# Kernel tuning notes

Hardware: AMD Instinct MI355X
Metric: run time of the kernel (lower is better)

Reference implementation:

```python
import jax, jax.numpy as jnp
import numpy as np

B, CIN, COUT, T, H, W, NH = 8, 16, 16, 32, 16, 16, 4
DIN = CIN * H * W    # 4096
DOUT = COUT * H * W  # 4096
DH = DOUT // NH      # 1024


def conv3d(x, w, b, pad):
    y = jax.lax.conv_general_dilated(
        x, w, window_strides=(1, 1, 1), padding=((pad, pad),) * 3,
        dimension_numbers=('NCDHW', 'OIDHW', 'NCDHW'))
    return y + b[None, :, None, None, None]


def instance_norm(x, eps=1e-5):
    # InstanceNorm3d default: no affine, normalize per (B,C) over (T,H,W)
    mu = x.mean(axis=(2, 3, 4), keepdims=True)
    var = ((x - mu) ** 2).mean(axis=(2, 3, 4), keepdims=True)
    return (x - mu) * jax.lax.rsqrt(var + eps)


def slstm(x, Wg, bg, Rg):
    # x: (B,T,D). Wg: (4,D,D) input weights [i,f,z,o]; bg: (4,D);
    # Rg: (NH,4,DH,DH) block-diagonal per-head recurrent weights.
    Bb, Tt, D = x.shape
    Gx = jnp.einsum('btd,god->btgo', x, Wg) + bg  # (B,T,4,D)

    def step(carry, gx):
        h, c, n, m = carry
        hh = h.reshape(Bb, NH, DH)
        gh = jnp.einsum('bhd,hgod->bhgo', hh, Rg)          # (B,NH,4,DH)
        pre = gx + gh.transpose(0, 2, 1, 3).reshape(Bb, 4, D)
        i_pre, f_pre, z_pre, o_pre = pre[:, 0], pre[:, 1], pre[:, 2], pre[:, 3]
        # stabilized exponential gating (xLSTM sLSTM)
        m_new = jnp.maximum(f_pre + m, i_pre)
        i = jnp.exp(i_pre - m_new)
        f = jnp.exp(f_pre + m - m_new)
        c = f * c + i * jnp.tanh(z_pre)
        n = f * n + i
        h = jax.nn.sigmoid(o_pre) * c / n
        return (h, c, n, m_new), h

    init = tuple(jnp.zeros((Bb, D), x.dtype) for _ in range(4))
    _, hs = jax.lax.scan(step, init, Gx.transpose(1, 0, 2, 3))  # hs: (T,B,D)
    return hs.transpose(1, 0, 2)


def setup_inputs():
    key = jax.random.key(0)
    ks = jax.random.split(key, 8)
    s = 0.02
    return {
        'x': jax.random.normal(ks[0], (B, CIN, T, H, W), jnp.float32),
        'c1_w': jax.random.normal(ks[1], (COUT, CIN, 3, 3, 3), jnp.float32) * 0.05,
        'c1_b': jnp.zeros((COUT,), jnp.float32),
        'c2_w': jax.random.normal(ks[2], (COUT, COUT, 3, 3, 3), jnp.float32) * 0.05,
        'c2_b': jnp.zeros((COUT,), jnp.float32),
        'c3_w': jax.random.normal(ks[3], (COUT, COUT, 3, 3, 3), jnp.float32) * 0.05,
        'c3_b': jnp.zeros((COUT,), jnp.float32),
        'pre_w': jax.random.normal(ks[4], (DOUT, DIN), jnp.float32) * s,
        'pre_b': jnp.zeros((DOUT,), jnp.float32),
        'lstm_W': jax.random.normal(ks[5], (4, DOUT, DOUT), jnp.float32) * s,
        'lstm_b': jnp.zeros((4, DOUT), jnp.float32),
        'lstm_R': jax.random.normal(ks[6], (NH, 4, DH, DH), jnp.float32) * s,
        'attn_w': jax.random.normal(ks[7], (1, 2 * COUT), jnp.float32) * 0.05,
        'attn_b': jnp.zeros((1,), jnp.float32),
    }


def reference(x, c1_w, c1_b, c2_w, c2_b, c3_w, c3_b, pre_w, pre_b,
              lstm_W, lstm_b, lstm_R, attn_w, attn_b):
    # conv3d branch: conv -> IN -> relu -> conv -> relu -> conv -> relu
    y = jax.nn.relu(instance_norm(conv3d(x, c1_w, c1_b, 1)))
    y = jax.nn.relu(conv3d(y, c2_w, c2_b, 1))
    out3d = jax.nn.relu(conv3d(y, c3_w, c3_b, 1))
    # sLSTM branch
    xs = x.transpose(0, 2, 1, 3, 4).reshape(B, T, DIN)
    xs = xs @ pre_w.T + pre_b
    hs = slstm(xs, lstm_W, lstm_b, lstm_R)                 # (B,T,DOUT)
    s_out = hs.reshape(B, T, COUT, H, W).transpose(0, 2, 1, 3, 4)
    # attention-gated fusion: cat -> 1x1x1 conv -> sigmoid -> weighted sum
    comb = jnp.concatenate([s_out, out3d], axis=1)         # (B,2*COUT,T,H,W)
    alpha = jax.nn.sigmoid(jnp.einsum('bcthw,oc->bothw', comb, attn_w)
                           + attn_b[None, :, None, None, None])
    return alpha * out3d + (1 - alpha) * s_out
```

## Files before the change

kernel.cpp:

```cpp
#include <hip/hip_runtime.h>
#include <hip/hip_bf16.h>
#include <cstddef>

#define BB   8
#define CIN  16
#define COUT 16
#define TT   32
#define HH   16
#define WW   16
#define DIN  4096
#define DOUT 4096
#define NH   4
#define DH   1024
#define SPAT 8192
#define NSEQ 256

typedef __attribute__((ext_vector_type(8))) short  bf16x8;
typedef __attribute__((ext_vector_type(4))) float  f32x4;
typedef __attribute__((ext_vector_type(4))) unsigned short us4;
typedef __attribute__((ext_vector_type(4))) int    i32x4;
typedef unsigned short ushort_t;
typedef unsigned long long u64_t;

static __device__ __forceinline__ ushort_t f2bf(float f) {
    union { float f; unsigned u; } v; v.f = f;
    unsigned r = (v.u + 0x7fffu + ((v.u >> 16) & 1u)) >> 16;
    return (ushort_t)r;
}
static __device__ __forceinline__ float bf2f(ushort_t u) {
    union { unsigned u; float f; } v; v.u = ((unsigned)u) << 16;
    return v.f;
}

__global__ void setup_kernel(const float* __restrict__ x, ushort_t* __restrict__ xt,
                             const float* __restrict__ w1, const float* __restrict__ w2,
                             const float* __restrict__ w3,
                             float* __restrict__ cw1, float* __restrict__ cw2,
                             float* __restrict__ cw3, int* __restrict__ flags) {
    int bid = blockIdx.x;
    if (bid < 1024) {
        int idx = bid * 256 + threadIdx.x;
        int n = idx >> 10, k4 = (idx & 1023) * 4;
        int b = n >> 5, t = n & 31, c = k4 >> 8, hw = k4 & 255;
        f32x4 f = *(const f32x4*)&x[(((size_t)(b * CIN + c) * TT + t)) * 256 + hw];
        us4 o;
        #pragma unroll
        for (int i = 0; i < 4; ++i) o[i] = f2bf(f[i]);
        *(us4*)&xt[(size_t)n * DIN + k4] = o;
    } else if (bid < 1105) {
        int i = (bid - 1024) * 256 + threadIdx.x;
        if (i < 3 * 6912) {
            int set = i / 6912, j = i - set * 6912;
            const float* w = (set == 0) ? w1 : (set == 1) ? w2 : w3;
            float* cw      = (set == 0) ? cw1 : (set == 1) ? cw2 : cw3;
            int o = j & 15, r = j >> 4;
            int k = r % 27, ci = r / 27;
            cw[j] = w[(size_t)(o * CIN + ci) * 27 + k];
        }
    } else {
        int j = (bid - 1105) * 256 + threadIdx.x;
        ((i32x4*)flags)[j] = (i32x4){0, 0, 0, 0};
    }
}

template<int BN, int BK, bool OUT_BF16, bool ADD_BIAS>
__global__ __launch_bounds__(256, 2)
void mfma_gemm_kernel(const ushort_t* __restrict__ A, const float* __restrict__ B,
                      const float* __restrict__ bias, void* __restrict__ C,
                      int N, int K) {
    constexpr int NF  = BN / 16;
    constexpr int TPR = 256 / BN;
    constexpr int FPT = BK / TPR;
    constexpr int RPI = 512 / BK;
    constexpr int LPR = 64 / RPI;
    __shared__ ushort_t Al[2][256][BK];
    __shared__ ushort_t Bl[2][BN][BK];
    int tid  = threadIdx.x;
    int lane = tid & 63;
    int wv   = tid >> 6;
    int n0 = blockIdx.x * BN;
    int ksp = K / gridDim.y;
    int kS  = blockIdx.y * ksp;

    f32x4 acc[4][NF];
    #pragma unroll
    for (int i = 0; i < 4; ++i)
        #pragma unroll
        for (int j = 0; j < NF; ++j) acc[i][j] = (f32x4){0.f, 0.f, 0.f, 0.f};

    auto stageA = [&](int buf, int k0) {
        #pragma unroll
        for (int q = 0; q < BK / 8; ++q) {
            int rbase = wv * 64 + q * RPI;
            int row = rbase + lane / LPR;
            const ushort_t* g = A + (size_t)row * K + k0 + (lane % LPR) * 8;
            __builtin_amdgcn_global_load_lds(
                (const __attribute__((address_space(1))) void*)g,
                (__attribute__((address_space(3))) void*)&Al[buf][rbase][0],
                16, 0, 0);
        }
    };
    auto stageB = [&](int buf, int k0) {
        int r  = tid / TPR;
        int cs = (tid % TPR) * FPT;
        const float* g = B + (size_t)(n0 + r) * K + k0 + cs;
        #pragma unroll
        for (int q = 0; q < FPT / 4; ++q) {
            f32x4 f = *(const f32x4*)(g + q * 4);
            us4 pk;
            #pragma unroll
            for (int e = 0; e < 4; ++e) pk[e] = f2bf(f[e]);
            *(us4*)&Bl[buf][r][cs + q * 4] = pk;
        }
    };
    auto compute = [&](int buf) {
        #pragma unroll
        for (int ks = 0; ks < BK / 32; ++ks) {
            bf16x8 af[4], bfr[NF];
            #pragma unroll
            for (int i = 0; i < 4; ++i)
                af[i] = *(const bf16x8*)&Al[buf][wv * 64 + i * 16 + (lane & 15)][ks * 32 + (lane >> 4) * 8];
            #pragma unroll
            for (int j = 0; j < NF; ++j)
                bfr[j] = *(const bf16x8*)&Bl[buf][j * 16 + (lane & 15)][ks * 32 + (lane >> 4) * 8];
            #pragma unroll
            for (int i = 0; i < 4; ++i)
                #pragma unroll
                for (int j = 0; j < NF; ++j)
                    acc[i][j] = __builtin_amdgcn_mfma_f32_16x16x32_bf16(af[i], bfr[j], acc[i][j], 0, 0, 0);
        }
    };

    stageA(0, kS); stageB(0, kS);
    __syncthreads();
    int nk = ksp / BK;
    int cur = 0;
    for (int t = 0; t < nk; ++t) {
        if (t + 1 < nk) { stageA(cur ^ 1, kS + (t + 1) * BK); stageB(cur ^ 1, kS + (t + 1) * BK); }
        compute(cur);
        __syncthreads();
        cur ^= 1;
    }

    size_t cofs = (size_t)blockIdx.y * 256 * N;
    #pragma unroll
    for (int i = 0; i < 4; ++i) {
        int row = wv * 64 + i * 16 + (lane >> 4) * 4;
        #pragma unroll
        for (int j = 0; j < NF; ++j) {
            int col = n0 + j * 16 + (lane & 15);
            float bv = ADD_BIAS ? bias[col] : 0.f;
            #pragma unroll
            for (int r = 0; r < 4; ++r) {
                float v = acc[i][j][r] + bv;
                if constexpr (OUT_BF16) ((ushort_t*)C)[cofs + (size_t)(row + r) * N + col] = f2bf(v);
                else                    ((float*)C)[cofs + (size_t)(row + r) * N + col] = v;
            }
        }
    }
}

#define GXPS ((size_t)NSEQ * 4 * DOUT)

__global__ __launch_bounds__(256, 1)
void lstm_persist_kernel(const float* __restrict__ R,
                         const float* __restrict__ Gx,
                         const float* __restrict__ lstm_b,
                         unsigned* __restrict__ hfr,
                         int* __restrict__ flags) {
    __shared__ ushort_t Rl[4][32][64 * 8];
    __shared__ float gh_p[4][4][16][8];

    int tid  = threadIdx.x;
    int lane = tid & 63;
    int w    = tid >> 6;
    int head = blockIdx.x >> 6;
    int oc   = blockIdx.x & 63;

    #pragma unroll 4
    for (int n = 0; n < 64; ++n) {
        int g = n >> 4, r = n & 15;
        const float* src = R + ((size_t)((head * 4 + g) * DH + oc * 16 + r)) * DH + tid * 4;
        f32x4 f = *(const f32x4*)src;
        int k0 = tid * 4;
        int ks = k0 >> 5;
        int kI = (k0 >> 3) & 3;
        int e8 = k0 & 7;
        union { ushort_t u[4]; u64_t q; } pk;
        #pragma unroll
        for (int e = 0; e < 4; ++e) pk.u[e] = f2bf(f[e]);
        *(u64_t*)&Rl[g][ks][((kI << 4) | r) * 8 + e8] = pk.q;
    }

    int arow = lane & 15;
    int part = arow >> 3;
    int bb   = arow & 7;
    int kseg = lane >> 4;

    int gb  = tid >> 4;
    int gol = tid & 15;
    int gd  = head * DH + oc * 16 + gol;
    int o_h = oc * 16 + gol;
    unsigned hslot = ((unsigned)head * 32 + (o_h >> 5)) * 256 + gb * 32 + (o_h & 31);
    float c_r = 0.f, n_r = 0.f, m_r = 0.f;
    float lb0 = 0.f, lb1 = 0.f, lb2 = 0.f, lb3 = 0.f;
    if (tid < 128) {
        lb0 = lstm_b[gd];
        lb1 = lstm_b[DOUT + gd];
        lb2 = lstm_b[2 * DOUT + gd];
        lb3 = lstm_b[3 * DOUT + gd];
    }

    __syncthreads();

    for (int t = 0; t < TT; ++t) {
        float gx0 = lb0, gx1 = lb1, gx2 = lb2, gx3 = lb3;
        if (tid < 128) {
            size_t gxoff = ((size_t)(gb * TT + t)) * (4 * DOUT) + gd;
            #pragma unroll
            for (int p = 0; p < 4; ++p) {
                const float* gp = Gx + p * GXPS + gxoff;
                gx0 += gp[0];
                gx1 += gp[DOUT];
                gx2 += gp[2 * DOUT];
                gx3 += gp[3 * DOUT];
            }
        }

        if (t > 0) {
            const int* fl = flags + (((t - 1) * 4 + head) << 6);
            for (;;) {
                int v = __hip_atomic_load(fl + lane, __ATOMIC_RELAXED,
                                          __HIP_MEMORY_SCOPE_AGENT);
                if (__all(v != 0)) break;
            }

            const u64_t* hb = (const u64_t*)hfr
                + ((((size_t)(t - 1) * 4 + head) * 32) * 256 + bb * 32 + kseg * 8) / 2;
            bf16x8 hf[8];
            #pragma unroll
            for (int j = 0; j < 8; ++j) {
                const u64_t* p = hb + (size_t)(w * 8 + j) * 128;
                union { ushort_t u[8]; bf16x8 v; } fr;
                #pragma unroll
                for (int e2 = 0; e2 < 4; ++e2) {
                    u64_t q = __hip_atomic_load(p + e2, __ATOMIC_RELAXED,
                                                __HIP_MEMORY_SCOPE_AGENT);
                    unsigned q0 = (unsigned)q, q1 = (unsigned)(q >> 32);
                    fr.u[e2 * 2]     = part ? (ushort_t)(q0 >> 16) : (ushort_t)(q0 & 0xffffu);
                    fr.u[e2 * 2 + 1] = part ? (ushort_t)(q1 >> 16) : (ushort_t)(q1 & 0xffffu);
                }
                hf[j] = fr.v;
            }

            f32x4 acc[4];
            #pragma unroll
            for (int g = 0; g < 4; ++g) acc[g] = (f32x4){0.f, 0.f, 0.f, 0.f};
            #pragma unroll
            for (int g = 0; g < 4; ++g)
                #pragma unroll
                for (int j = 0; j < 8; ++j) {
                    bf16x8 a = *(const bf16x8*)&Rl[g][w * 8 + j][lane * 8];
                    acc[g] = __builtin_amdgcn_mfma_f32_16x16x32_bf16(a, hf[j], acc[g], 0, 0, 0);
                }
            #pragma unroll
            for (int g = 0; g < 4; ++g)
                #pragma unroll
                for (int r = 0; r < 4; ++r)
                    acc[g][r] += __shfl_xor(acc[g][r], 8, 64);
            if (part == 0) {
                int orow0 = kseg * 4;
                #pragma unroll
                for (int g = 0; g < 4; ++g)
                    #pragma unroll
                    for (int r = 0; r < 4; ++r)
                        gh_p[w][g][orow0 + r][bb] = acc[g][r];
            }
        } else {
            for (int i = tid; i < 4 * 4 * 16 * 8; i += 256)
                ((float*)gh_p)[i] = 0.f;
        }
        __syncthreads();

        if (tid < 128) {
            float ip = gx0 +
                gh_p[0][0][gol][gb] + gh_p[1][0][gol][gb] + gh_p[2][0][gol][gb] + gh_p[3][0][gol][gb];
            float fp = gx1 +
                gh_p[0][1][gol][gb] + gh_p[1][1][gol][gb] + gh_p[2][1][gol][gb] + gh_p[3][1][gol][gb];
            float zp = gx2 +
                gh_p[0][2][gol][gb] + gh_p[1][2][gol][gb] + gh_p[2][2][gol][gb] + gh_p[3][2][gol][gb];
            float op = gx3 +
                gh_p[0][3][gol][gb] + gh_p[1][3][gol][gb] + gh_p[2][3][gol][gb] + gh_p[3][3][gol][gb];
            float mn = fmaxf(fp + m_r, ip);
            float iv = __expf(ip - mn);
            float fv = __expf(fp + m_r - mn);
            float zc = fminf(fmaxf(zp, -9.f), 9.f);
            float th = 1.f - 2.f / (__expf(2.f * zc) + 1.f);
            c_r = fv * c_r + iv * th;
            n_r = fv * n_r + iv;
            float sig = 1.f / (1.f + __expf(-op));
            float hv = sig * c_r / n_r;
            m_r = mn;
            unsigned hi = f2bf(hv);
            unsigned lo = f2bf(hv - bf2f((ushort_t)hi));
            __hip_atomic_store(&hfr[(size_t)t * 32768 + hslot],
                               hi | (lo << 16),
                               __ATOMIC_RELAXED, __HIP_MEMORY_SCOPE_AGENT);
        }
        __syncthreads();
        if (tid == 0)
            __hip_atomic_store(&flags[((t * 4 + head) << 6) + oc], 1,
                               __ATOMIC_RELAXED, __HIP_MEMORY_SCOPE_AGENT);
    }
}

template<bool NORM, bool PSUM>
__global__ __launch_bounds__(256)
void conv3d_kernel(const float* __restrict__ in, const float* __restrict__ cw,
                   const float* __restrict__ bias, const float* __restrict__ stats,
                   float* __restrict__ out, float* __restrict__ psum, int relu) {
    __shared__ float xin[CIN][3][256];
    int blk = blockIdx.x;
    int b = blk >> 6, t = (blk >> 1) & 31, half = blk & 1;
    int tid = threadIdx.x;

    for (int i = tid; i < CIN * 3 * 256; i += 256) {
        int hw = i & 255, r = i >> 8;
        int kt = r % 3, ci = r / 3;
        int tt = t + kt - 1;
        float v = 0.f;
        if ((unsigned)tt < TT) {
            v = in[((size_t)(b * CIN + ci) * TT + tt) * 256 + hw];
            if constexpr (NORM) {
                float mu = stats[(b * CIN + ci) * 2];
                float rs = stats[(b * CIN + ci) * 2 + 1];
                v = fmaxf((v - mu) * rs, 0.f);
            }
        }
        xin[ci][kt][hw] = v;
    }
    __syncthreads();

    int h = tid >> 4, wx = tid & 15;
    f32x4 a0 = *(const f32x4*)&bias[half * 8];
    f32x4 a1 = *(const f32x4*)&bias[half * 8 + 4];

    for (int ci = 0; ci < CIN; ++ci) {
        #pragma unroll
        for (int kt = 0; kt < 3; ++kt) {
            #pragma unroll
            for (int kh = 0; kh < 3; ++kh) {
                int h2 = h + kh - 1;
                bool vh = (unsigned)h2 < HH;
                int h2c = vh ? h2 : 0;
                #pragma unroll
                for (int kw = 0; kw < 3; ++kw) {
                    int w2 = wx + kw - 1;
                    bool v = vh && ((unsigned)w2 < WW);
                    int w2c = ((unsigned)w2 < WW) ? w2 : 0;
                    float xv = xin[ci][kt][h2c * 16 + w2c];
                    xv = v ? xv : 0.f;
                    const float* wp = cw + (size_t)(ci * 27 + kt * 9 + kh * 3 + kw) * 16 + half * 8;
                    f32x4 w0 = *(const f32x4*)(wp);
                    f32x4 w1 = *(const f32x4*)(wp + 4);
                    a0 += xv * w0; a1 += xv * w1;
                }
            }
        }
    }
    float accs[8];
    #pragma unroll
    for (int i = 0; i < 4; ++i) { accs[i] = a0[i]; accs[4 + i] = a1[i]; }
    #pragma unroll
    for (int o = 0; o < 8; ++o) {
        float v = accs[o];
        if (relu) v = fmaxf(v, 0.f);
        out[((size_t)(b * COUT + half * 8 + o) * TT + t) * 256 + tid] = v;
    }

    if constexpr (PSUM) {
        __syncthreads();
        float* sm = (float*)xin;
        int wv = tid >> 6;
        #pragma unroll
        for (int o = 0; o < 8; ++o) {
            float s = accs[o];
            float q = accs[o] * accs[o];
            #pragma unroll
            for (int m = 1; m < 64; m <<= 1) {
                s += __shfl_xor(s, m, 64);
                q += __shfl_xor(q, m, 64);
            }
            if ((tid & 63) == 0) { sm[wv * 16 + o * 2] = s; sm[wv * 16 + o * 2 + 1] = q; }
        }
        __syncthreads();
        if (tid < 16) {
            int o = tid >> 1, which = tid & 1;
            float v = sm[o * 2 + which] + sm[16 + o * 2 + which]
                    + sm[32 + o * 2 + which] + sm[48 + o * 2 + which];
            psum[((((size_t)(b * 32 + t) * 2 + half) * 8 + o) * 2) + which] = v;
        }
    }
}

__global__ void inorm_stats_kernel(const float* __restrict__ psum, float* __restrict__ stats) {
    int tid = threadIdx.x;
    if (tid < 128) {
        int b = tid >> 4, c = tid & 15;
        int half = c >> 3, ch = c & 7;
        float sum = 0.f, sq = 0.f;
        for (int t = 0; t < TT; ++t) {
            size_t base = (((size_t)(b * 32 + t) * 2 + half) * 8 + ch) * 2;
            sum += psum[base];
            sq  += psum[base + 1];
        }
        float mu = sum / (float)SPAT;
        float var = sq / (float)SPAT - mu * mu;
        stats[(b * CIN + c) * 2]     = mu;
        stats[(b * CIN + c) * 2 + 1] = rsqrtf(var + 1e-5f);
    }
}

__global__ void combine_kernel(const unsigned* __restrict__ hfr,
                               const float* __restrict__ out3d,
                               const float* __restrict__ attn_w,
                               const float* __restrict__ attn_b,
                               float* __restrict__ out) {
    int idx = blockIdx.x * 256 + threadIdx.x;
    int hw = idx & 255;
    int t  = (idx >> 8) & 31;
    int b  = idx >> 13;
    float dot = attn_b[0];
    float sv[16], ov[16];
    #pragma unroll
    for (int ch = 0; ch < 16; ++ch) {
        int d = ch * 256 + hw;
        int head = d >> 10, o_h = d & 1023;
        size_t slot = (size_t)t * 32768 + (size_t)head * 8192
                    + (o_h >> 5) * 256 + b * 32 + (o_h & 31);
        unsigned v32 = hfr[slot];
        float s = bf2f((ushort_t)(v32 & 0xffffu)) + bf2f((ushort_t)(v32 >> 16));
        float o3 = out3d[(((size_t)(b * COUT + ch) * TT + t)) * 256 + hw];
        sv[ch] = s; ov[ch] = o3;
        dot += attn_w[ch] * s + attn_w[16 + ch] * o3;
    }
    float alpha = 1.f / (1.f + expf(-dot));
    #pragma unroll
    for (int ch = 0; ch < 16; ++ch) {
        out[(((size_t)(b * COUT + ch) * TT + t)) * 256 + hw] =
            alpha * ov[ch] + (1.f - alpha) * sv[ch];
    }
}

extern "C" void kernel_launch(void* const* d_in, const int* in_sizes, int n_in,
                              void* d_out, int out_size, void* d_ws, size_t ws_size,
                              hipStream_t stream) {
    const float* x      = (const float*)d_in[0];
    const float* c1_w   = (const float*)d_in[1];
    const float* c1_b   = (const float*)d_in[2];
    const float* c2_w   = (const float*)d_in[3];
    const float* c2_b   = (const float*)d_in[4];
    const float* c3_w   = (const float*)d_in[5];
    const float* c3_b   = (const float*)d_in[6];
    const float* pre_w  = (const float*)d_in[7];
    const float* pre_b  = (const float*)d_in[8];
    const float* lstm_W = (const float*)d_in[9];
    const float* lstm_b = (const float*)d_in[10];
    const float* lstm_R = (const float*)d_in[11];
    const float* attn_w = (const float*)d_in[12];
    const float* attn_b = (const float*)d_in[13];
    float* out = (float*)d_out;

    float* wsf = (float*)d_ws;
    float* y1    = wsf;
    float* y2    = y1 + 1048576;
    float* out3d = y2 + 1048576;
    float* Gx    = out3d + 1048576;
    float* cw1   = Gx + 4 * 4194304;
    float* cw2   = cw1 + 6912;
    float* cw3   = cw2 + 6912;
    float* stats = cw3 + 6912;
    float* psum  = stats + 256;
    float* pad   = psum + 8192;
    ushort_t* xt   = (ushort_t*)(pad + 64);
    ushort_t* xs2b = xt + 1048576;
    unsigned* hfr  = (unsigned*)(xs2b + 1048576);
    int*     flags = (int*)(hfr + 1048576);

    setup_kernel<<<1113, 256, 0, stream>>>(x, xt, c1_w, c2_w, c3_w, cw1, cw2, cw3, flags);

    conv3d_kernel<false, true><<<512, 256, 0, stream>>>(x, cw1, c1_b, nullptr, y1, psum, 0);
    inorm_stats_kernel<<<1, 256, 0, stream>>>(psum, stats);
    conv3d_kernel<true, false><<<512, 256, 0, stream>>>(y1, cw2, c2_b, stats, y2, nullptr, 1);
    conv3d_kernel<false, false><<<512, 256, 0, stream>>>(y2, cw3, c3_b, nullptr, out3d, nullptr, 1);

    mfma_gemm_kernel<16, 64, true, true><<<dim3(DOUT / 16, 1), 256, 0, stream>>>(
        xt, pre_w, pre_b, xs2b, DOUT, DIN);
    mfma_gemm_kernel<32, 64, false, false><<<dim3(4 * DOUT / 32, 4), 256, 0, stream>>>(
        xs2b, lstm_W, nullptr, Gx, 4 * DOUT, DOUT);

    lstm_persist_kernel<<<256, 256, 0, stream>>>(lstm_R, Gx, lstm_b, hfr, flags);

    combine_kernel<<<256, 256, 0, stream>>>(hfr, out3d, attn_w, attn_b, out);
}
```

Baseline: 603.4 us.

## Co-schedule conv blocks with GEMM blocks in fused kernels and halve Gx split-K

```diff
diff --git a/kernel.cpp b/kernel.cpp
--- a/kernel.cpp
+++ b/kernel.cpp
@@ -64,23 +64,22 @@
 }
 
 template<int BN, int BK, bool OUT_BF16, bool ADD_BIAS>
-__global__ __launch_bounds__(256, 2)
-void mfma_gemm_kernel(const ushort_t* __restrict__ A, const float* __restrict__ B,
-                      const float* __restrict__ bias, void* __restrict__ C,
-                      int N, int K) {
+__device__ __forceinline__
+void gemm_body(char* smem, int bx, int by, int nsplit,
+               const ushort_t* __restrict__ A, const float* __restrict__ B,
+               const float* __restrict__ bias, void* __restrict__ C,
+               int N, int K) {
     constexpr int NF  = BN / 16;
     constexpr int TPR = 256 / BN;
     constexpr int FPT = BK / TPR;
-    constexpr int RPI = 512 / BK;
-    constexpr int LPR = 64 / RPI;
-    __shared__ ushort_t Al[2][256][BK];
-    __shared__ ushort_t Bl[2][BN][BK];
+    ushort_t* Al = (ushort_t*)smem;
+    ushort_t* Bl = Al + 2 * 256 * BK;
     int tid  = threadIdx.x;
     int lane = tid & 63;
     int wv   = tid >> 6;
-    int n0 = blockIdx.x * BN;
-    int ksp = K / gridDim.y;
-    int kS  = blockIdx.y * ksp;
+    int n0 = bx * BN;
+    int ksp = K / nsplit;
+    int kS  = by * ksp;
 
     f32x4 acc[4][NF];
     #pragma unroll
@@ -90,13 +89,13 @@
 
     auto stageA = [&](int buf, int k0) {
         #pragma unroll
-        for (int q = 0; q < BK / 8; ++q) {
-            int rbase = wv * 64 + q * RPI;
-            int row = rbase + lane / LPR;
-            const ushort_t* g = A + (size_t)row * K + k0 + (lane % LPR) * 8;
+        for (int q = 0; q < 8; ++q) {
+            int rbase = wv * 64 + q * 8;
+            int row = rbase + (lane >> 3);
+            const ushort_t* g = A + (size_t)row * K + k0 + (lane & 7) * 8;
             __builtin_amdgcn_global_load_lds(
                 (const __attribute__((address_space(1))) void*)g,
-                (__attribute__((address_space(3))) void*)&Al[buf][rbase][0],
+                (__attribute__((address_space(3))) void*)&Al[(buf * 256 + rbase) * BK],
                 16, 0, 0);
         }
     };
@@ -110,7 +109,7 @@
             us4 pk;
             #pragma unroll
             for (int e = 0; e < 4; ++e) pk[e] = f2bf(f[e]);
-            *(us4*)&Bl[buf][r][cs + q * 4] = pk;
+            *(us4*)&Bl[(buf * BN + r) * BK + cs + q * 4] = pk;
         }
     };
     auto compute = [&](int buf) {
@@ -119,10 +118,10 @@
             bf16x8 af[4], bfr[NF];
             #pragma unroll
             for (int i = 0; i < 4; ++i)
-                af[i] = *(const bf16x8*)&Al[buf][wv * 64 + i * 16 + (lane & 15)][ks * 32 + (lane >> 4) * 8];
+                af[i] = *(const bf16x8*)&Al[(buf * 256 + wv * 64 + i * 16 + (lane & 15)) * BK + ks * 32 + (lane >> 4) * 8];
             #pragma unroll
             for (int j = 0; j < NF; ++j)
-                bfr[j] = *(const bf16x8*)&Bl[buf][j * 16 + (lane & 15)][ks * 32 + (lane >> 4) * 8];
+                bfr[j] = *(const bf16x8*)&Bl[(buf * BN + j * 16 + (lane & 15)) * BK + ks * 32 + (lane >> 4) * 8];
             #pragma unroll
             for (int i = 0; i < 4; ++i)
                 #pragma unroll
@@ -142,7 +141,7 @@
         cur ^= 1;
     }
 
-    size_t cofs = (size_t)blockIdx.y * 256 * N;
+    size_t cofs = (size_t)by * 256 * N;
     #pragma unroll
     for (int i = 0; i < 4; ++i) {
         int row = wv * 64 + i * 16 + (lane >> 4) * 4;
@@ -157,6 +156,147 @@
                 else                    ((float*)C)[cofs + (size_t)(row + r) * N + col] = v;
             }
         }
+    }
+}
+
+template<bool NORM, bool PSUM>
+__device__ __forceinline__
+void conv_body(char* smem, int blk,
+               const float* __restrict__ in, const float* __restrict__ cw,
+               const float* __restrict__ bias, const float* __restrict__ stats,
+               float* __restrict__ out, float* __restrict__ psum, int relu) {
+    float* xin = (float*)smem;
+    int b = blk >> 6, t = (blk >> 1) & 31, half = blk & 1;
+    int tid = threadIdx.x;
+
+    for (int i = tid; i < CIN * 3 * 256; i += 256) {
+        int hw = i & 255, r = i >> 8;
+        int kt = r % 3, ci = r / 3;
+        int tt = t + kt - 1;
+        float v = 0.f;
+        if ((unsigned)tt < TT) {
+            v = in[((size_t)(b * CIN + ci) * TT + tt) * 256 + hw];
+            if constexpr (NORM) {
+                float mu = stats[(b * CIN + ci) * 2];
+                float rs = stats[(b * CIN + ci) * 2 + 1];
+                v = fmaxf((v - mu) * rs, 0.f);
+            }
+        }
+        xin[(ci * 3 + kt) * 256 + hw] = v;
+    }
+    __syncthreads();
+
+    int h = tid >> 4, wx = tid & 15;
+    f32x4 a0 = *(const f32x4*)&bias[half * 8];
+    f32x4 a1 = *(const f32x4*)&bias[half * 8 + 4];
+
+    for (int ci = 0; ci < CIN; ++ci) {
+        #pragma unroll
+        for (int kt = 0; kt < 3; ++kt) {
+            #pragma unroll
+            for (int kh = 0; kh < 3; ++kh) {
+                int h2 = h + kh - 1;
+                bool vh = (unsigned)h2 < HH;
+                int h2c = vh ? h2 : 0;
+                #pragma unroll
+                for (int kw = 0; kw < 3; ++kw) {
+                    int w2 = wx + kw - 1;
+                    bool v = vh && ((unsigned)w2 < WW);
+                    int w2c = ((unsigned)w2 < WW) ? w2 : 0;
+                    float xv = xin[(ci * 3 + kt) * 256 + h2c * 16 + w2c];
+                    xv = v ? xv : 0.f;
+                    const float* wp = cw + (size_t)(ci * 27 + kt * 9 + kh * 3 + kw) * 16 + half * 8;
+                    f32x4 w0 = *(const f32x4*)(wp);
+                    f32x4 w1 = *(const f32x4*)(wp + 4);
+                    a0 += xv * w0; a1 += xv * w1;
+                }
+            }
+        }
+    }
+    float accs[8];
+    #pragma unroll
+    for (int i = 0; i < 4; ++i) { accs[i] = a0[i]; accs[4 + i] = a1[i]; }
+    #pragma unroll
+    for (int o = 0; o < 8; ++o) {
+        float v = accs[o];
+        if (relu) v = fmaxf(v, 0.f);
+        out[((size_t)(b * COUT + half * 8 + o) * TT + t) * 256 + tid] = v;
+    }
+
+    if constexpr (PSUM) {
+        __syncthreads();
+        float* sm = xin;
+        int wv = tid >> 6;
+        #pragma unroll
+        for (int o = 0; o < 8; ++o) {
+            float s = accs[o];
+            float q = accs[o] * accs[o];
+            #pragma unroll
+            for (int m = 1; m < 64; m <<= 1) {
+                s += __shfl_xor(s, m, 64);
+                q += __shfl_xor(q, m, 64);
+            }
+            if ((tid & 63) == 0) { sm[wv * 16 + o * 2] = s; sm[wv * 16 + o * 2 + 1] = q; }
+        }
+        __syncthreads();
+        if (tid < 16) {
+            int o = tid >> 1, which = tid & 1;
+            float v = sm[o * 2 + which] + sm[16 + o * 2 + which]
+                    + sm[32 + o * 2 + which] + sm[48 + o * 2 + which];
+            psum[((((size_t)(b * 32 + t) * 2 + half) * 8 + o) * 2) + which] = v;
+        }
+    }
+}
+
+__global__ __launch_bounds__(256, 2)
+void fused1_kernel(const ushort_t* __restrict__ xt, const float* __restrict__ pre_w,
+                   const float* __restrict__ pre_b, ushort_t* __restrict__ xs2b,
+                   const float* __restrict__ x, const float* __restrict__ cw1,
+                   const float* __restrict__ c1_b, float* __restrict__ y1,
+                   float* __restrict__ psum) {
+    extern __shared__ char smem[];
+    if (blockIdx.x < 256)
+        gemm_body<16, 64, true, true>(smem, blockIdx.x, 0, 1, xt, pre_w, pre_b, xs2b, DOUT, DIN);
+    else
+        conv_body<false, true>(smem, blockIdx.x - 256, x, cw1, c1_b, nullptr, y1, psum, 0);
+}
+
+__global__ __launch_bounds__(256, 2)
+void fused2_kernel(const ushort_t* __restrict__ xs2b, const float* __restrict__ lstm_W,
+                   float* __restrict__ Gx,
+                   const float* __restrict__ y1, const float* __restrict__ cw2,
+                   const float* __restrict__ c2_b, const float* __restrict__ stats,
+                   float* __restrict__ y2) {
+    extern __shared__ char smem[];
+    if (blockIdx.x < 1024)
+        gemm_body<32, 64, false, false>(smem, blockIdx.x & 511, blockIdx.x >> 9, 2,
+                                        xs2b, lstm_W, nullptr, Gx, 4 * DOUT, DOUT);
+    else
+        conv_body<true, false>(smem, blockIdx.x - 1024, y1, cw2, c2_b, stats, y2, nullptr, 1);
+}
+
+__global__ __launch_bounds__(256, 2)
+void conv3_kernel(const float* __restrict__ y2, const float* __restrict__ cw3,
+                  const float* __restrict__ c3_b, float* __restrict__ out3d) {
+    extern __shared__ char smem[];
+    conv_body<false, false>(smem, blockIdx.x, y2, cw3, c3_b, nullptr, out3d, nullptr, 1);
+}
+
+__global__ void inorm_stats_kernel(const float* __restrict__ psum, float* __restrict__ stats) {
+    int tid = threadIdx.x;
+    if (tid < 128) {
+        int b = tid >> 4, c = tid & 15;
+        int half = c >> 3, ch = c & 7;
+        float sum = 0.f, sq = 0.f;
+        for (int t = 0; t < TT; ++t) {
+            size_t base = (((size_t)(b * 32 + t) * 2 + half) * 8 + ch) * 2;
+            sum += psum[base];
+            sq  += psum[base + 1];
+        }
+        float mu = sum / (float)SPAT;
+        float var = sq / (float)SPAT - mu * mu;
+        stats[(b * CIN + c) * 2]     = mu;
+        stats[(b * CIN + c) * 2 + 1] = rsqrtf(var + 1e-5f);
     }
 }
 
@@ -218,7 +358,7 @@
         if (tid < 128) {
             size_t gxoff = ((size_t)(gb * TT + t)) * (4 * DOUT) + gd;
             #pragma unroll
-            for (int p = 0; p < 4; ++p) {
+            for (int p = 0; p < 2; ++p) {
                 const float* gp = Gx + p * GXPS + gxoff;
                 gx0 += gp[0];
                 gx1 += gp[DOUT];
@@ -233,6 +373,7 @@
                 int v = __hip_atomic_load(fl + lane, __ATOMIC_RELAXED,
                                           __HIP_MEMORY_SCOPE_AGENT);
                 if (__all(v != 0)) break;
+                __builtin_amdgcn_s_sleep(1);
             }
 
             const u64_t* hb = (const u64_t*)hfr
@@ -314,113 +455,6 @@
     }
 }
 
-template<bool NORM, bool PSUM>
-__global__ __launch_bounds__(256)
-void conv3d_kernel(const float* __restrict__ in, const float* __restrict__ cw,
-                   const float* __restrict__ bias, const float* __restrict__ stats,
-                   float* __restrict__ out, float* __restrict__ psum, int relu) {
-    __shared__ float xin[CIN][3][256];
-    int blk = blockIdx.x;
-    int b = blk >> 6, t = (blk >> 1) & 31, half = blk & 1;
-    int tid = threadIdx.x;
-
-    for (int i = tid; i < CIN * 3 * 256; i += 256) {
-        int hw = i & 255, r = i >> 8;
-        int kt = r % 3, ci = r / 3;
-        int tt = t + kt - 1;
-        float v = 0.f;
-        if ((unsigned)tt < TT) {
-            v = in[((size_t)(b * CIN + ci) * TT + tt) * 256 + hw];
-            if constexpr (NORM) {
-                float mu = stats[(b * CIN + ci) * 2];
-                float rs = stats[(b * CIN + ci) * 2 + 1];
-                v = fmaxf((v - mu) * rs, 0.f);
-            }
-        }
-        xin[ci][kt][hw] = v;
-    }
-    __syncthreads();
-
-    int h = tid >> 4, wx = tid & 15;
-    f32x4 a0 = *(const f32x4*)&bias[half * 8];
-    f32x4 a1 = *(const f32x4*)&bias[half * 8 + 4];
-
-    for (int ci = 0; ci < CIN; ++ci) {
-        #pragma unroll
-        for (int kt = 0; kt < 3; ++kt) {
-            #pragma unroll
-            for (int kh = 0; kh < 3; ++kh) {
-                int h2 = h + kh - 1;
-                bool vh = (unsigned)h2 < HH;
-                int h2c = vh ? h2 : 0;
-                #pragma unroll
-                for (int kw = 0; kw < 3; ++kw) {
-                    int w2 = wx + kw - 1;
-                    bool v = vh && ((unsigned)w2 < WW);
-                    int w2c = ((unsigned)w2 < WW) ? w2 : 0;
-                    float xv = xin[ci][kt][h2c * 16 + w2c];
-                    xv = v ? xv : 0.f;
-                    const float* wp = cw + (size_t)(ci * 27 + kt * 9 + kh * 3 + kw) * 16 + half * 8;
-                    f32x4 w0 = *(const f32x4*)(wp);
-                    f32x4 w1 = *(const f32x4*)(wp + 4);
-                    a0 += xv * w0; a1 += xv * w1;
-                }
-            }
-        }
-    }
-    float accs[8];
-    #pragma unroll
-    for (int i = 0; i < 4; ++i) { accs[i] = a0[i]; accs[4 + i] = a1[i]; }
-    #pragma unroll
-    for (int o = 0; o < 8; ++o) {
-        float v = accs[o];
-        if (relu) v = fmaxf(v, 0.f);
-        out[((size_t)(b * COUT + half * 8 + o) * TT + t) * 256 + tid] = v;
-    }
-
-    if constexpr (PSUM) {
-        __syncthreads();
-        float* sm = (float*)xin;
-        int wv = tid >> 6;
-        #pragma unroll
-        for (int o = 0; o < 8; ++o) {
-            float s = accs[o];
-            float q = accs[o] * accs[o];
-            #pragma unroll
-            for (int m = 1; m < 64; m <<= 1) {
-                s += __shfl_xor(s, m, 64);
-                q += __shfl_xor(q, m, 64);
-            }
-            if ((tid & 63) == 0) { sm[wv * 16 + o * 2] = s; sm[wv * 16 + o * 2 + 1] = q; }
-        }
-        __syncthreads();
-        if (tid < 16) {
-            int o = tid >> 1, which = tid & 1;
-            float v = sm[o * 2 + which] + sm[16 + o * 2 + which]
-                    + sm[32 + o * 2 + which] + sm[48 + o * 2 + which];
-            psum[((((size_t)(b * 32 + t) * 2 + half) * 8 + o) * 2) + which] = v;
-        }
-    }
-}
-
-__global__ void inorm_stats_kernel(const float* __restrict__ psum, float* __restrict__ stats) {
-    int tid = threadIdx.x;
-    if (tid < 128) {
-        int b = tid >> 4, c = tid & 15;
-        int half = c >> 3, ch = c & 7;
-        float sum = 0.f, sq = 0.f;
-        for (int t = 0; t < TT; ++t) {
-            size_t base = (((size_t)(b * 32 + t) * 2 + half) * 8 + ch) * 2;
-            sum += psum[base];
-            sq  += psum[base + 1];
-        }
-        float mu = sum / (float)SPAT;
-        float var = sq / (float)SPAT - mu * mu;
-        stats[(b * CIN + c) * 2]     = mu;
-        stats[(b * CIN + c) * 2 + 1] = rsqrtf(var + 1e-5f);
-    }
-}
-
 __global__ void combine_kernel(const unsigned* __restrict__ hfr,
                                const float* __restrict__ out3d,
                                const float* __restrict__ attn_w,
@@ -476,7 +510,7 @@
     float* y2    = y1 + 1048576;
     float* out3d = y2 + 1048576;
     float* Gx    = out3d + 1048576;
-    float* cw1   = Gx + 4 * 4194304;
+    float* cw1   = Gx + 2 * 4194304;
     float* cw2   = cw1 + 6912;
     float* cw3   = cw2 + 6912;
     float* stats = cw3 + 6912;
@@ -489,15 +523,14 @@
 
     setup_kernel<<<1113, 256, 0, stream>>>(x, xt, c1_w, c2_w, c3_w, cw1, cw2, cw3, flags);
 
-    conv3d_kernel<false, true><<<512, 256, 0, stream>>>(x, cw1, c1_b, nullptr, y1, psum, 0);
+    fused1_kernel<<<768, 256, 69632, stream>>>(xt, pre_w, pre_b, xs2b,
+                                               x, cw1, c1_b, y1, psum);
     inorm_stats_kernel<<<1, 256, 0, stream>>>(psum, stats);
-    conv3d_kernel<true, false><<<512, 256, 0, stream>>>(y1, cw2, c2_b, stats, y2, nullptr, 1);
-    conv3d_kernel<false, false><<<512, 256, 0, stream>>>(y2, cw3, c3_b, nullptr, out3d, nullptr, 1);
-
-    mfma_gemm_kernel<16, 64, true, true><<<dim3(DOUT / 16, 1), 256, 0, stream>>>(
-        xt, pre_w, pre_b, xs2b, DOUT, DIN);
-    mfma_gemm_kernel<32, 64, false, false><<<dim3(4 * DOUT / 32, 4), 256, 0, stream>>>(
-        xs2b, lstm_W, nullptr, Gx, 4 * DOUT, DOUT);
+
+    fused2_kernel<<<1536, 256, 73728, stream>>>(xs2b, lstm_W, Gx,
+                                                y1, cw2, c2_b, stats, y2);
+
+    conv3_kernel<<<512, 256, 49152, stream>>>(y2, cw3, c3_b, out3d);
 
     lstm_persist_kernel<<<256, 256, 0, stream>>>(lstm_R, Gx, lstm_b, hfr, flags);
 
```

Result: faster. 531.4 us (-11.9%).
